# Kernel tuning notes

Measured on AMD Instinct MI355X. Metric: run time of the kernel, lower is better.

Reference implementation:

```python
import jax, jax.numpy as jnp
import numpy as np

BANK_FILTERS = 64
DIM = 128
KSIZE = 3
BATCH = 256


def setup_inputs() -> dict:
    key = jax.random.key(0)
    k1, k2 = jax.random.split(key)
    bank_request = jax.random.normal(k1, (BATCH, BANK_FILTERS), dtype=jnp.float32)
    weight = jax.random.normal(k2, (BANK_FILTERS, DIM, DIM, KSIZE, KSIZE), dtype=jnp.float32)
    return {"bank_request": bank_request, "weight": weight}


def reference(bank_request, weight):
    # softmax over filter bank, then weighted sum of filters -> per-sample kernel
    probs = jax.nn.softmax(bank_request, axis=1)          # (B, F)
    Fb, D1, D2, K1, K2 = weight.shape
    # express as a single GEMM over the filter axis instead of broadcast-mul-reduce
    w2d = weight.reshape(Fb, D1 * D2 * K1 * K2)           # (F, D*D*k*k)
    kernel = probs @ w2d                                   # (B, D*D*k*k)
    return kernel.reshape(bank_request.shape[0], D1, D2, K1, K2)
```

## Files before the change

### kernel.cpp

```cpp
#include <hip/hip_runtime.h>
#include <math.h>

#define BATCH 256
#define FB    64
#define NCOL  147456
#define TPB   256
#define BT    32

#define FMA4(a, s, w) do { \
    (a).x = fmaf((s), (w).x, (a).x); \
    (a).y = fmaf((s), (w).y, (a).y); \
    (a).z = fmaf((s), (w).z, (a).z); \
    (a).w = fmaf((s), (w).w, (a).w); \
} while (0)

__global__ void softmax_rows(const float* __restrict__ x, float* __restrict__ p) {
    const int b = blockIdx.x;
    const int lane = threadIdx.x;
    float v = x[b * FB + lane];
    float m = v;
#pragma unroll
    for (int o = 32; o > 0; o >>= 1) m = fmaxf(m, __shfl_xor(m, o));
    float e = __expf(v - m);
    float s = e;
#pragma unroll
    for (int o = 32; o > 0; o >>= 1) s += __shfl_xor(s, o);
    p[b * FB + lane] = e / s;
}

__global__ __launch_bounds__(TPB, 2) void bank_gemm(
        const float* __restrict__ W, const float* __restrict__ P,
        float* __restrict__ out) {
    __shared__ float pt[FB * BT];

    const int tid = threadIdx.x;
    const int bg  = blockIdx.y;

    for (int i = tid; i < FB * BT; i += TPB) {
        const int f = i & (FB - 1);
        const int b = i >> 6;
        pt[f * BT + b] = P[bg * (FB * BT) + i];
    }
    __syncthreads();

    const int ncol4 = NCOL / 4;
    const float4* Wv = (const float4*)W;
    const int c4 = blockIdx.x * TPB + tid;

    float4 acc[BT];
#pragma unroll
    for (int b = 0; b < BT; ++b) acc[b] = make_float4(0.f, 0.f, 0.f, 0.f);

    float4 w = Wv[c4];
    for (int f = 0; f < FB; ++f) {
        float4 wn = w;
        if (f + 1 < FB) wn = Wv[(f + 1) * ncol4 + c4];
        const float4* p4 = (const float4*)&pt[f * BT];
#pragma unroll
        for (int q = 0; q < BT / 4; ++q) {
            const float4 p = p4[q];
            FMA4(acc[4 * q + 0], p.x, w);
            FMA4(acc[4 * q + 1], p.y, w);
            FMA4(acc[4 * q + 2], p.z, w);
            FMA4(acc[4 * q + 3], p.w, w);
        }
        w = wn;
    }

    float4* Ov = (float4*)out;
    const long long obase = (long long)(bg * BT) * ncol4 + c4;
#pragma unroll
    for (int b = 0; b < BT; ++b) {
        Ov[obase + (long long)b * ncol4] = acc[b];
    }
}

extern "C" void kernel_launch(void* const* d_in, const int* in_sizes, int n_in,
                              void* d_out, int out_size, void* d_ws, size_t ws_size,
                              hipStream_t stream) {
    const float* bank   = (const float*)d_in[0];
    const float* weight = (const float*)d_in[1];
    float* out   = (float*)d_out;
    float* probs = (float*)d_ws;

    softmax_rows<<<BATCH, FB, 0, stream>>>(bank, probs);

    dim3 grid(NCOL / (TPB * 4), BATCH / BT);
    bank_gemm<<<grid, TPB, 0, stream>>>(weight, probs, out);
}
```

Measured before the change: 218.7 us.

## Replace FP32 FMA GEMM with split-bf16 MFMA and XCD-aware block remap

Rewrites the bank GEMM to use 16x16x32 bf16 MFMA instructions, splitting both probabilities and weights into high and low bf16 parts and using three products to keep near-FP32 accuracy. Block indices are remapped so the batch groups sharing a column tile land on the same XCD to reuse weight data in L2. This trades vector FMA throughput for matrix-core throughput at the cost of extra conversion work and narrower, scalar output stores.

```diff
diff --git a/kernel.cpp b/kernel.cpp
--- a/kernel.cpp
+++ b/kernel.cpp
@@ -5,14 +5,20 @@
 #define FB    64
 #define NCOL  147456
 #define TPB   256
-#define BT    32
+#define MT    32
+#define NTB   512
+#define NXB   (NCOL / NTB)
+#define NBG   (BATCH / MT)
 
-#define FMA4(a, s, w) do { \
-    (a).x = fmaf((s), (w).x, (a).x); \
-    (a).y = fmaf((s), (w).y, (a).y); \
-    (a).z = fmaf((s), (w).z, (a).z); \
-    (a).w = fmaf((s), (w).w, (a).w); \
-} while (0)
+typedef __attribute__((ext_vector_type(8))) short bf16x8;
+typedef __attribute__((ext_vector_type(4))) float f32x4;
+
+__device__ __forceinline__ short bhi(float x) {
+    return (short)(__float_as_uint(x) >> 16);
+}
+__device__ __forceinline__ float fhi(float x) {
+    return __uint_as_float(__float_as_uint(x) & 0xffff0000u);
+}
 
 __global__ void softmax_rows(const float* __restrict__ x, float* __restrict__ p) {
     const int b = blockIdx.x;
@@ -28,51 +34,86 @@
     p[b * FB + lane] = e / s;
 }
 
-__global__ __launch_bounds__(TPB, 2) void bank_gemm(
+__global__ __launch_bounds__(TPB, 2) void bank_gemm_mfma(
         const float* __restrict__ W, const float* __restrict__ P,
         float* __restrict__ out) {
-    __shared__ float pt[FB * BT];
+    const int tid  = threadIdx.x;
+    const int wv   = tid >> 6;
+    const int lane = tid & 63;
+    const int kg   = lane >> 4;
+    const int lr   = lane & 15;
 
-    const int tid = threadIdx.x;
-    const int bg  = blockIdx.y;
+    const int wg   = blockIdx.y * gridDim.x + blockIdx.x;
+    const int xcd  = wg & 7;
+    const int slot = wg >> 3;
+    const int bx   = xcd * (NXB / 8) + (slot >> 3);
+    const int bg   = slot & (NBG - 1);
 
-    for (int i = tid; i < FB * BT; i += TPB) {
-        const int f = i & (FB - 1);
-        const int b = i >> 6;
-        pt[f * BT + b] = P[bg * (FB * BT) + i];
-    }
-    __syncthreads();
+    const int row0 = bg * MT;
+    const int col0 = bx * NTB + wv * 128;
 
-    const int ncol4 = NCOL / 4;
-    const float4* Wv = (const float4*)W;
-    const int c4 = blockIdx.x * TPB + tid;
-
-    float4 acc[BT];
+    bf16x8 pah[2][2], pal[2][2];
 #pragma unroll
-    for (int b = 0; b < BT; ++b) acc[b] = make_float4(0.f, 0.f, 0.f, 0.f);
-
-    float4 w = Wv[c4];
-    for (int f = 0; f < FB; ++f) {
-        float4 wn = w;
-        if (f + 1 < FB) wn = Wv[(f + 1) * ncol4 + c4];
-        const float4* p4 = (const float4*)&pt[f * BT];
+    for (int rt = 0; rt < 2; ++rt) {
 #pragma unroll
-        for (int q = 0; q < BT / 4; ++q) {
-            const float4 p = p4[q];
-            FMA4(acc[4 * q + 0], p.x, w);
-            FMA4(acc[4 * q + 1], p.y, w);
-            FMA4(acc[4 * q + 2], p.z, w);
-            FMA4(acc[4 * q + 3], p.w, w);
+        for (int s = 0; s < 2; ++s) {
+            const float* pr = P + (row0 + rt * 16 + lr) * FB + s * 32 + kg * 8;
+            float av[8];
+            *(f32x4*)&av[0] = *(const f32x4*)pr;
+            *(f32x4*)&av[4] = *(const f32x4*)(pr + 4);
+#pragma unroll
+            for (int i = 0; i < 8; ++i) {
+                const float xx = av[i];
+                pah[rt][s][i] = bhi(xx);
+                pal[rt][s][i] = bhi(xx - fhi(xx));
+            }
         }
-        w = wn;
     }
 
-    float4* Ov = (float4*)out;
-    const long long obase = (long long)(bg * BT) * ncol4 + c4;
+    f32x4 acc[2][8];
 #pragma unroll
-    for (int b = 0; b < BT; ++b) {
-        Ov[obase + (long long)b * ncol4] = acc[b];
+    for (int rt = 0; rt < 2; ++rt)
+#pragma unroll
+        for (int t = 0; t < 8; ++t)
+            acc[rt][t] = (f32x4){0.f, 0.f, 0.f, 0.f};
+
+    const float* wbase = W + (kg * 8) * NCOL + col0 + lr;
+#pragma unroll
+    for (int t = 0; t < 8; ++t) {
+        const float* wp = wbase + t * 16;
+        float wv0[8], wv1[8];
+#pragma unroll
+        for (int i = 0; i < 8; ++i) {
+            wv0[i] = wp[i * NCOL];
+            wv1[i] = wp[(32 + i) * NCOL];
+        }
+        bf16x8 wh0, wl0, wh1, wl1;
+#pragma unroll
+        for (int i = 0; i < 8; ++i) {
+            wh0[i] = bhi(wv0[i]); wl0[i] = bhi(wv0[i] - fhi(wv0[i]));
+            wh1[i] = bhi(wv1[i]); wl1[i] = bhi(wv1[i] - fhi(wv1[i]));
+        }
+#pragma unroll
+        for (int rt = 0; rt < 2; ++rt) {
+            f32x4 c = acc[rt][t];
+            c = __builtin_amdgcn_mfma_f32_16x16x32_bf16(pah[rt][0], wh0, c, 0, 0, 0);
+            c = __builtin_amdgcn_mfma_f32_16x16x32_bf16(pah[rt][1], wh1, c, 0, 0, 0);
+            c = __builtin_amdgcn_mfma_f32_16x16x32_bf16(pah[rt][0], wl0, c, 0, 0, 0);
+            c = __builtin_amdgcn_mfma_f32_16x16x32_bf16(pah[rt][1], wl1, c, 0, 0, 0);
+            c = __builtin_amdgcn_mfma_f32_16x16x32_bf16(pal[rt][0], wh0, c, 0, 0, 0);
+            c = __builtin_amdgcn_mfma_f32_16x16x32_bf16(pal[rt][1], wh1, c, 0, 0, 0);
+            acc[rt][t] = c;
+        }
     }
+
+#pragma unroll
+    for (int rt = 0; rt < 2; ++rt)
+#pragma unroll
+        for (int t = 0; t < 8; ++t)
+#pragma unroll
+            for (int r = 0; r < 4; ++r)
+                out[(size_t)(row0 + rt * 16 + kg * 4 + r) * NCOL
+                    + col0 + t * 16 + lr] = acc[rt][t][r];
 }
 
 extern "C" void kernel_launch(void* const* d_in, const int* in_sizes, int n_in,
@@ -85,6 +126,6 @@
 
     softmax_rows<<<BATCH, FB, 0, stream>>>(bank, probs);
 
-    dim3 grid(NCOL / (TPB * 4), BATCH / BT);
-    bank_gemm<<<grid, TPB, 0, stream>>>(weight, probs, out);
+    dim3 grid(NXB, NBG);
+    bank_gemm_mfma<<<grid, TPB, 0, stream>>>(weight, probs, out);
 }
```

After: 205.1 us, median of 2. -6.2%, faster.
